# Kernel tuning notes

Measured on AMD Instinct MI355X. Metric: run time of the kernel, lower is better.

## Reference

```python
import jax, jax.numpy as jnp
import numpy as np

N_NODES = 50000
NUM_FEAT = 2000
HEADS = 8
HID = 8
NUM_CLASSES = 30
NUM_EDGES = 1_600_000
NEG_SLOPE = 0.2


def _segment_softmax(scores, seg, num_segments):
    # scores: [E, H], seg: [E] destination node ids
    m = jax.ops.segment_max(scores, seg, num_segments=num_segments)
    m = jnp.where(jnp.isfinite(m), m, 0.0)  # guard empty segments
    e = jnp.exp(scores - m[seg])
    s = jax.ops.segment_sum(e, seg, num_segments=num_segments)
    return e / (s[seg] + 1e-16)


def _gat_layer(x, src, dst, w, att_src, att_dst, bias, concat):
    # PyG GATConv (eval mode: dropout disabled). x: [N, F_in]
    n = x.shape[0]
    h_, c_ = att_src.shape
    h = (x @ w).reshape(n, h_, c_)                      # [N, H, C]
    a_src = (h * att_src[None]).sum(-1)                 # [N, H]
    a_dst = (h * att_dst[None]).sum(-1)                 # [N, H]
    alpha = jax.nn.leaky_relu(a_src[src] + a_dst[dst], NEG_SLOPE)  # [E, H]
    alpha = _segment_softmax(alpha, dst, n)             # per-dest softmax
    msg = h[src] * alpha[:, :, None]                    # [E, H, C]
    out = jax.ops.segment_sum(msg, dst, num_segments=n) # [N, H, C]
    out = out.reshape(n, h_ * c_) if concat else out.mean(axis=1)
    return out + bias, alpha


def _add_self_loops(edge_index, n):
    loops = jnp.arange(n, dtype=edge_index.dtype)
    src = jnp.concatenate([edge_index[0], loops])
    dst = jnp.concatenate([edge_index[1], loops])
    return src, dst


def setup_inputs() -> dict:
    key = jax.random.key(0)
    ks = jax.random.split(key, 12)
    x = jax.random.normal(ks[0], (N_NODES, NUM_FEAT), jnp.float32)
    edge_index = jax.random.randint(ks[1], (2, NUM_EDGES), 0, N_NODES, jnp.int32)
    d1 = HEADS * HID
    w_res = jax.random.normal(ks[2], (NUM_FEAT, d1), jnp.float32) / np.sqrt(NUM_FEAT)
    b_res = jnp.zeros((d1,), jnp.float32)
    w1 = jax.random.normal(ks[3], (NUM_FEAT, d1), jnp.float32) / np.sqrt(NUM_FEAT)
    att_src1 = jax.random.normal(ks[4], (HEADS, HID), jnp.float32) * 0.1
    att_dst1 = jax.random.normal(ks[5], (HEADS, HID), jnp.float32) * 0.1
    b1 = jnp.zeros((d1,), jnp.float32)
    w2 = jax.random.normal(ks[6], (d1, NUM_CLASSES), jnp.float32) / np.sqrt(d1)
    att_src2 = jax.random.normal(ks[7], (1, NUM_CLASSES), jnp.float32) * 0.1
    att_dst2 = jax.random.normal(ks[8], (1, NUM_CLASSES), jnp.float32) * 0.1
    b2 = jnp.zeros((NUM_CLASSES,), jnp.float32)
    return {"x": x, "edge_index": edge_index, "w_res": w_res, "b_res": b_res,
            "w1": w1, "att_src1": att_src1, "att_dst1": att_dst1, "b1": b1,
            "w2": w2, "att_src2": att_src2, "att_dst2": att_dst2, "b2": b2}


def reference(x, edge_index, w_res, b_res, w1, att_src1, att_dst1, b1,
              w2, att_src2, att_dst2, b2):
    n = x.shape[0]
    src, dst = _add_self_loops(edge_index, n)
    res = x @ w_res + b_res                                   # residual branch
    h1, alpha1 = _gat_layer(x, src, dst, w1, att_src1, att_dst1, b1, concat=True)
    x1 = jax.nn.elu(h1 + res)                                 # dropout = identity (eval)
    h2, alpha2 = _gat_layer(x1, src, dst, w2, att_src2, att_dst2, b2, concat=False)
    x2 = jax.nn.elu(h2)
    return jax.nn.log_softmax(x2, axis=1), alpha1, alpha2
```

## Files before the change

kernel.cpp:

```cpp
#include <hip/hip_runtime.h>
#include <hip/hip_bf16.h>

#define N_NODES 50000
#define NUM_FEAT 2000
#define HEADS 8
#define HID 8
#define NUM_CLASSES 30
#define NUM_EDGES 1600000
#define E_TOTAL (NUM_EDGES + N_NODES)
#define E8 (E_TOTAL * 8)
#define KT32 64
#define KT64 32
#define ROWCAP 128
#define LOG2E 1.44269504f
#define SENT N_NODES
#define NEG_BIG -1.0e30f

typedef __attribute__((ext_vector_type(8))) short short8;
typedef __attribute__((ext_vector_type(4))) float f32x4;

typedef __attribute__((address_space(1))) const unsigned int gu32;
typedef __attribute__((address_space(3))) unsigned int lu32;

__device__ __forceinline__ void gload_lds16(const void* g, void* l) {
  __builtin_amdgcn_global_load_lds((gu32*)g, (lu32*)l, 16, 0, 0);
}

__device__ __forceinline__ ushort f2bf(float f) {
  __hip_bfloat16 b = __float2bfloat16(f);
  return *reinterpret_cast<ushort*>(&b);
}

__device__ __forceinline__ float bf2f(ushort u) {
  unsigned int x = ((unsigned int)u) << 16;
  union { unsigned int i; float f; } c; c.i = x;
  return c.f;
}

__device__ __forceinline__ float lexp2(float sc) {
  return exp2f(fmaxf(sc, 0.2f * sc));
}

__device__ __forceinline__ short8 cvt8(float4 a, float4 b) {
  union { short8 v; ushort u[8]; } p;
  p.u[0] = f2bf(a.x); p.u[1] = f2bf(a.y); p.u[2] = f2bf(a.z); p.u[3] = f2bf(a.w);
  p.u[4] = f2bf(b.x); p.u[5] = f2bf(b.y); p.u[6] = f2bf(b.z); p.u[7] = f2bf(b.w);
  return p.v;
}

__global__ __launch_bounds__(256) void k_init(int* __restrict__ esrc,
    const float* __restrict__ Wres, const float* __restrict__ W1,
    ushort* __restrict__ Bp, int* __restrict__ cursor) {
  int i = blockIdx.x * 256 + threadIdx.x;
  if (i < N_NODES * ROWCAP / 4)
    *(int4*)&esrc[i * 4] = make_int4(SENT, SENT, SENT, SENT);
  if (i < N_NODES / 4)
    *(int4*)&cursor[i * 4] = make_int4(0, 0, 0, 0);
  if (i < KT32 * 4 * 128) {
    int col = i & 127;
    int kbase = (i >> 7) * 8;
    const float* W = (col < 64) ? Wres : W1;
    int c = col & 63;
    union { short8 v; ushort u[8]; } p;
#pragma unroll
    for (int j = 0; j < 8; ++j) {
      int k = kbase + j;
      p.u[j] = f2bf(k < NUM_FEAT ? W[(size_t)k * 64 + c] : 0.f);
    }
    *(short8*)&Bp[(size_t)i * 8] = p.v;
  }
}

__global__ __launch_bounds__(256) void k_gemm_mfma(const float* __restrict__ X,
    const ushort* __restrict__ Bp, const float* __restrict__ brs,
    const float* __restrict__ b1, float* __restrict__ Hres,
    ushort* __restrict__ Hatt) {
  __shared__ ushort ldsB[2][8192];
  const int tid = threadIdx.x;
  const int lane = tid & 63, wid = tid >> 6;
  const int lg = lane >> 4, lr = lane & 15;
  const int m0 = blockIdx.x * 64;

  int rowg = m0 + wid * 16 + lr;
  rowg = rowg < N_NODES ? rowg : N_NODES - 1;
  const float* axp = X + (size_t)rowg * NUM_FEAT + lg * 8;

  f32x4 acc[8] = {};
  float4 a[4], na[4];
  const float4 fz = make_float4(0.f, 0.f, 0.f, 0.f);

  auto loadA = [&](int t, float4* r) {
#pragma unroll
    for (int s = 0; s < 2; ++s) {
      int k0 = t * 64 + s * 32 + lg * 8;
      if (k0 < NUM_FEAT) {
        r[2 * s]     = *(const float4*)(axp + t * 64 + s * 32);
        r[2 * s + 1] = *(const float4*)(axp + t * 64 + s * 32 + 4);
      } else { r[2 * s] = fz; r[2 * s + 1] = fz; }
    }
  };
  auto dmaB = [&](int t, int buf) {
#pragma unroll
    for (int q = 0; q < 4; ++q) {
      const ushort* g = Bp + ((size_t)t * 1024 + q * 256 + wid * 64 + lane) * 8;
      gload_lds16(g, &ldsB[buf][(size_t)(q * 256 + wid * 64) * 8]);
    }
  };
  auto mfmaStep = [&](int cur, const float4* av) {
#pragma unroll
    for (int s = 0; s < 2; ++s) {
      short8 fb[8];
#pragma unroll
      for (int n = 0; n < 8; ++n)
        fb[n] = *(const short8*)&ldsB[cur][(size_t)(s * 512 + lg * 128 + n * 16 + lr) * 8];
      short8 fa = cvt8(av[2 * s], av[2 * s + 1]);
#pragma unroll
      for (int n = 0; n < 8; ++n)
        acc[n] = __builtin_amdgcn_mfma_f32_16x16x32_bf16(fa, fb[n], acc[n], 0, 0, 0);
    }
  };

  dmaB(0, 0);
  __builtin_amdgcn_sched_barrier(0);
  loadA(0, a);
  asm volatile("s_waitcnt vmcnt(4)" ::: "memory");
  __builtin_amdgcn_s_barrier();
  __builtin_amdgcn_sched_barrier(0);

  for (int t = 0; t < KT64 - 1; ++t) {
    const int cur = t & 1, nxt = cur ^ 1;
    dmaB(t + 1, nxt);
    __builtin_amdgcn_sched_barrier(0);
    loadA(t + 1, na);
    mfmaStep(cur, a);
    asm volatile("s_waitcnt vmcnt(4)" ::: "memory");
    __builtin_amdgcn_s_barrier();
    __builtin_amdgcn_sched_barrier(0);
#pragma unroll
    for (int q = 0; q < 4; ++q) a[q] = na[q];
  }
  mfmaStep((KT64 - 1) & 1, a);

#pragma unroll
  for (int n = 0; n < 8; ++n) {
    int col = n * 16 + lr;
    if (col < 64) {
      float badd = brs[col] + b1[col];
#pragma unroll
      for (int i = 0; i < 4; ++i) {
        int row = m0 + wid * 16 + lg * 4 + i;
        if (row < N_NODES) Hres[(size_t)row * 64 + col] = acc[n][i] + badd;
      }
    } else {
#pragma unroll
      for (int i = 0; i < 4; ++i) {
        int row = m0 + wid * 16 + lg * 4 + i;
        if (row < N_NODES) Hatt[(size_t)row * 64 + (col - 64)] = f2bf(acc[n][i]);
      }
    }
  }
}

__global__ void k_fill_attn(const int* __restrict__ ei, int* __restrict__ cursor,
                            int* __restrict__ esrc, ushort* __restrict__ Hatt,
                            const float* __restrict__ att_src,
                            const float* __restrict__ att_dst,
                            float* __restrict__ a_src, float2* __restrict__ dinv1) {
  int i = blockIdx.x * 256 + threadIdx.x;
  if (i < N_NODES * HEADS) {
    int h = i & 7;
    const ushort* hp = &Hatt[(size_t)(i >> 3) * 64 + h * 8];
    float s = 0.f, d = 0.f;
#pragma unroll
    for (int c = 0; c < 8; ++c) {
      float v = bf2f(hp[c]);
      s = fmaf(v, att_src[h * 8 + c], s);
      d = fmaf(v, att_dst[h * 8 + c], d);
    }
    a_src[i] = s * LOG2E;
    dinv1[i] = make_float2(d * LOG2E, 0.f);
  }
  if (i < E_TOTAL) {
    int s, d;
    if (i < NUM_EDGES) { s = ei[i]; d = ei[NUM_EDGES + i]; }
    else { s = d = i - NUM_EDGES; }
    int pos = atomicAdd(&cursor[d], 1);
    esrc[(unsigned)(d * ROWCAP + pos)] = s;
  }
  if (i < 64) Hatt[(size_t)SENT * 64 + i] = 0;
  if (i >= 64 && i < 72) a_src[SENT * 8 + (i - 64)] = NEG_BIG;
}

__global__ __launch_bounds__(256) void k_layer1f(const int* __restrict__ esrc,
    const int* __restrict__ cursor,
    const float* __restrict__ Hres, const ushort* __restrict__ Hatt,
    const float* __restrict__ a_src, float2* __restrict__ dinv1,
    const float* __restrict__ w2, const float* __restrict__ att_src2,
    const float* __restrict__ att_dst2, ushort* __restrict__ h2b,
    float* __restrict__ a_src2, float2* __restrict__ dinv2) {
  __shared__ float w2s[64 * 30];
  __shared__ float xs[4][64];
  for (int i = threadIdx.x; i < 64 * 30; i += 256) w2s[i] = w2[i];
  if (blockIdx.x == 0) {
    if (threadIdx.x < 32) h2b[(unsigned)(SENT * 32 + threadIdx.x)] = 0;
    if (threadIdx.x == 32) a_src2[SENT] = NEG_BIG;
  }
  __syncthreads();
  int wave = threadIdx.x >> 6, lane = threadIdx.x & 63;
  int n = blockIdx.x * 4 + wave;
  if (n >= N_NODES) return;
  int hd = lane >> 3;
  float adn = dinv1[(unsigned)(n * 8 + hd)].x;
  int start = n * ROWCAP, end = start + ((cursor[n] + 7) & ~7);
  float denom = 0.f, msg = 0.f;
  for (int p = start; p < end; p += 8) {
    int4 v0 = *(const int4*)&esrc[p];
    int4 v1 = *(const int4*)&esrc[p + 4];
    int s8[8] = {v0.x, v0.y, v0.z, v0.w, v1.x, v1.y, v1.z, v1.w};
    float av[8];
    ushort hu[8];
#pragma unroll
    for (int i = 0; i < 8; ++i) {
      av[i] = a_src[(unsigned)(s8[i] * 8 + hd)];
      hu[i] = Hatt[(unsigned)(s8[i] * 64 + lane)];
    }
#pragma unroll
    for (int i = 0; i < 8; ++i) {
      float ev = lexp2(av[i] + adn);
      denom += ev;
      msg = fmaf(ev, bf2f(hu[i]), msg);
    }
  }
  float invd = 1.f / (denom + 1e-16f);
  float x1v = msg * invd + Hres[(unsigned)(n * 64 + lane)];
  x1v = x1v > 0.f ? x1v : __expf(x1v) - 1.f;
  if ((lane & 7) == 0) dinv1[(unsigned)(n * 8 + hd)].y = invd;

  xs[wave][lane] = x1v;
  float acc2 = 0.f;
  if (lane < 30) {
#pragma unroll 8
    for (int k = 0; k < 64; ++k) acc2 = fmaf(xs[wave][k], w2s[k * 30 + lane], acc2);
  }
  float as = (lane < 30) ? acc2 * att_src2[lane] : 0.f;
  float ad = (lane < 30) ? acc2 * att_dst2[lane] : 0.f;
  for (int off = 1; off < 64; off <<= 1) {
    as += __shfl_xor(as, off);
    ad += __shfl_xor(ad, off);
  }
  if (lane == 0) { a_src2[n] = as * LOG2E; dinv2[n] = make_float2(ad * LOG2E, 0.f); }
  if (lane < 32) h2b[(unsigned)(n * 32 + lane)] = (lane < 30) ? f2bf(acc2) : (ushort)0;
}

__global__ __launch_bounds__(256) void k_layer2(const int* __restrict__ esrc,
    const int* __restrict__ cursor,
    const ushort* __restrict__ h2b, const float* __restrict__ a_src2,
    float2* __restrict__ dinv2, const float* __restrict__ b2,
    float* __restrict__ out0) {
  int wave = threadIdx.x >> 6, lane = threadIdx.x & 63;
  int n = blockIdx.x * 4 + wave;
  if (n >= N_NODES) return;
  float adn = dinv2[n].x;
  int start = n * ROWCAP, end = start + ((cursor[n] + 7) & ~7);
  int half = lane >> 5, cls = lane & 31;
  float denom = 0.f, msg = 0.f;
  for (int p = start; p < end; p += 4) {
    int s0 = esrc[p + half];
    int s1 = esrc[p + 2 + half];
    float as0 = a_src2[(unsigned)s0], as1 = a_src2[(unsigned)s1];
    ushort hv0 = h2b[(unsigned)(s0 * 32 + cls)];
    ushort hv1 = h2b[(unsigned)(s1 * 32 + cls)];
    float ev0 = lexp2(as0 + adn);
    denom += ev0;
    msg = fmaf(ev0, bf2f(hv0), msg);
    float ev1 = lexp2(as1 + adn);
    denom += ev1;
    msg = fmaf(ev1, bf2f(hv1), msg);
  }
  denom += __shfl_xor(denom, 32);
  msg   += __shfl_xor(msg, 32);
  float invd = 1.f / (denom + 1e-16f);
  bool act = lane < 30;
  float o = act ? msg * invd + b2[lane] : 0.f;
  float x2 = o > 0.f ? o : __expf(o) - 1.f;
  float mv = act ? x2 : -1e30f;
  for (int off = 1; off < 64; off <<= 1) mv = fmaxf(mv, __shfl_xor(mv, off));
  float ex = act ? __expf(x2 - mv) : 0.f;
  for (int off = 1; off < 64; off <<= 1) ex += __shfl_xor(ex, off);
  if (act) out0[(size_t)n * 30 + lane] = x2 - mv - __logf(ex);
  if (lane == 0) dinv2[n].y = invd;
}

__global__ __launch_bounds__(256) void k_alpha(const int* __restrict__ ei,
    const float* __restrict__ a_src1, const float2* __restrict__ dinv1,
    const float* __restrict__ a_src2, const float2* __restrict__ dinv2,
    float* __restrict__ alpha1, float* __restrict__ alpha2) {
  int i = blockIdx.x * 256 + threadIdx.x;
  if (i >= E8) return;
  {
    int e = i >> 3, h = i & 7;
    int s, d;
    if (e < NUM_EDGES) { s = ei[e]; d = ei[NUM_EDGES + e]; }
    else { s = d = e - NUM_EDGES; }
    float2 di = dinv1[(unsigned)(d * 8 + h)];
    alpha1[i] = lexp2(a_src1[(unsigned)(s * 8 + h)] + di.x) * di.y;
  }
  if (i < E_TOTAL) {
    int s, d;
    if (i < NUM_EDGES) { s = ei[i]; d = ei[NUM_EDGES + i]; }
    else { s = d = i - NUM_EDGES; }
    float2 dj = dinv2[(unsigned)d];
    alpha2[i] = lexp2(a_src2[(unsigned)s] + dj.x) * dj.y;
  }
}

extern "C" void kernel_launch(void* const* d_in, const int* in_sizes, int n_in,
                              void* d_out, int out_size, void* d_ws, size_t ws_size,
                              hipStream_t stream) {
  const float* x        = (const float*)d_in[0];
  const int*   ei       = (const int*)d_in[1];
  const float* w_res    = (const float*)d_in[2];
  const float* b_res    = (const float*)d_in[3];
  const float* w1       = (const float*)d_in[4];
  const float* att_src1 = (const float*)d_in[5];
  const float* att_dst1 = (const float*)d_in[6];
  const float* b1       = (const float*)d_in[7];
  const float* w2       = (const float*)d_in[8];
  const float* att_src2 = (const float*)d_in[9];
  const float* att_dst2 = (const float*)d_in[10];
  const float* b2       = (const float*)d_in[11];

  float* ws = (float*)d_ws;
  float* Hres    = ws;
  float* a_src1  = Hres + (size_t)N_NODES * 64;
  float2* dinv1  = (float2*)(a_src1 + (size_t)(N_NODES + 1) * 8);
  float* a_src2  = (float*)(dinv1 + (size_t)N_NODES * 8);
  float2* dinv2  = (float2*)(a_src2 + N_NODES + 1);
  ushort* Hatt   = (ushort*)(dinv2 + N_NODES);
  ushort* h2b    = Hatt + (size_t)(N_NODES + 1) * 64;
  ushort* Bp     = h2b + (size_t)(N_NODES + 1) * 32 + 32;
  int*   cursor  = (int*)(Bp + (size_t)KT32 * 4096 + 64);

  float* out0   = (float*)d_out;
  float* alpha1 = out0 + (size_t)N_NODES * 30;
  float* alpha2 = alpha1 + (size_t)E8;
  int*   esrc   = (int*)alpha1;

  k_init<<<(N_NODES * ROWCAP / 4 + 255) / 256, 256, 0, stream>>>(esrc, w_res, w1,
                                                                 Bp, cursor);
  k_gemm_mfma<<<(N_NODES + 63) / 64, 256, 0, stream>>>(x, Bp, b_res, b1, Hres, Hatt);
  k_fill_attn<<<(E_TOTAL + 255) / 256, 256, 0, stream>>>(ei, cursor, esrc, Hatt,
                                                         att_src1, att_dst1,
                                                         a_src1, dinv1);
  k_layer1f<<<(N_NODES + 3) / 4, 256, 0, stream>>>(esrc, cursor, Hres, Hatt,
                                                   a_src1, dinv1, w2, att_src2,
                                                   att_dst2, h2b, a_src2, dinv2);
  k_layer2<<<(N_NODES + 3) / 4, 256, 0, stream>>>(esrc, cursor, h2b, a_src2,
                                                  dinv2, b2, out0);
  k_alpha<<<(E8 + 255) / 256, 256, 0, stream>>>(ei, a_src1, dinv1, a_src2, dinv2,
                                                alpha1, alpha2);
}
```

Measured before the change: 432.0 us.

## Overlap edge CSR fill with the input GEMM in one launch

Moves the atomic edge-bucketing work (cursor atomics and esrc scatter) out of the attention-score kernel and into extra blocks appended to the GEMM launch. The memory-bound GEMM and the atomic-bound fill can then run on the GPU at the same time, instead of the fill waiting for the GEMM to finish. The attention-score kernel now launches over only N*HEADS threads. Fill blocks still declare the GEMM's large LDS allocation, which may limit how many of them can be resident at once, and they compete with GEMM blocks for bandwidth.

```diff
diff --git a/kernel.cpp b/kernel.cpp
--- a/kernel.cpp
+++ b/kernel.cpp
@@ -12,6 +12,8 @@
 #define KT32 64
 #define KT64 32
 #define ROWCAP 128
+#define GEMM_BLOCKS ((N_NODES + 63) / 64)
+#define FILL_BLOCKS ((E_TOTAL + 255) / 256)
 #define LOG2E 1.44269504f
 #define SENT N_NODES
 #define NEG_BIG -1.0e30f
@@ -71,11 +73,23 @@
   }
 }
 
-__global__ __launch_bounds__(256) void k_gemm_mfma(const float* __restrict__ X,
+__global__ __launch_bounds__(256) void k_gemm_fill(const float* __restrict__ X,
     const ushort* __restrict__ Bp, const float* __restrict__ brs,
     const float* __restrict__ b1, float* __restrict__ Hres,
-    ushort* __restrict__ Hatt) {
+    ushort* __restrict__ Hatt, const int* __restrict__ ei,
+    int* __restrict__ cursor, int* __restrict__ esrc) {
   __shared__ ushort ldsB[2][8192];
+  if (blockIdx.x >= GEMM_BLOCKS) {
+    int e = (blockIdx.x - GEMM_BLOCKS) * 256 + threadIdx.x;
+    if (e < E_TOTAL) {
+      int s, d;
+      if (e < NUM_EDGES) { s = ei[e]; d = ei[NUM_EDGES + e]; }
+      else { s = d = e - NUM_EDGES; }
+      int pos = atomicAdd(&cursor[d], 1);
+      esrc[(unsigned)(d * ROWCAP + pos)] = s;
+    }
+    return;
+  }
   const int tid = threadIdx.x;
   const int lane = tid & 63, wid = tid >> 6;
   const int lg = lane >> 4, lr = lane & 15;
@@ -161,11 +175,10 @@
   }
 }
 
-__global__ void k_fill_attn(const int* __restrict__ ei, int* __restrict__ cursor,
-                            int* __restrict__ esrc, ushort* __restrict__ Hatt,
-                            const float* __restrict__ att_src,
-                            const float* __restrict__ att_dst,
-                            float* __restrict__ a_src, float2* __restrict__ dinv1) {
+__global__ void k_attn1(ushort* __restrict__ Hatt,
+                        const float* __restrict__ att_src,
+                        const float* __restrict__ att_dst,
+                        float* __restrict__ a_src, float2* __restrict__ dinv1) {
   int i = blockIdx.x * 256 + threadIdx.x;
   if (i < N_NODES * HEADS) {
     int h = i & 7;
@@ -179,13 +192,6 @@
     }
     a_src[i] = s * LOG2E;
     dinv1[i] = make_float2(d * LOG2E, 0.f);
-  }
-  if (i < E_TOTAL) {
-    int s, d;
-    if (i < NUM_EDGES) { s = ei[i]; d = ei[NUM_EDGES + i]; }
-    else { s = d = i - NUM_EDGES; }
-    int pos = atomicAdd(&cursor[d], 1);
-    esrc[(unsigned)(d * ROWCAP + pos)] = s;
   }
   if (i < 64) Hatt[(size_t)SENT * 64 + i] = 0;
   if (i >= 64 && i < 72) a_src[SENT * 8 + (i - 64)] = NEG_BIG;
@@ -348,10 +354,12 @@
 
   k_init<<<(N_NODES * ROWCAP / 4 + 255) / 256, 256, 0, stream>>>(esrc, w_res, w1,
                                                                  Bp, cursor);
-  k_gemm_mfma<<<(N_NODES + 63) / 64, 256, 0, stream>>>(x, Bp, b_res, b1, Hres, Hatt);
-  k_fill_attn<<<(E_TOTAL + 255) / 256, 256, 0, stream>>>(ei, cursor, esrc, Hatt,
-                                                         att_src1, att_dst1,
-                                                         a_src1, dinv1);
+  k_gemm_fill<<<GEMM_BLOCKS + FILL_BLOCKS, 256, 0, stream>>>(x, Bp, b_res, b1,
+                                                             Hres, Hatt, ei,
+                                                             cursor, esrc);
+  k_attn1<<<(N_NODES * HEADS + 255) / 256, 256, 0, stream>>>(Hatt, att_src1,
+                                                             att_dst1, a_src1,
+                                                             dinv1);
   k_layer1f<<<(N_NODES + 3) / 4, 256, 0, stream>>>(esrc, cursor, Hres, Hatt,
                                                    a_src1, dinv1, w2, att_src2,
                                                    att_dst2, h2b, a_src2, dinv2);
```

Result: faster. 374.8 us (-13.2%).
